# Kernel optimization log

Hardware: AMD Instinct MI355X
Metric: run time of the kernel (lower is better)

The kernel has to match this reference:

```python
import jax, jax.numpy as jnp
import numpy as np

N_CH, LONG, LAT = 8, 64, 64
N = N_CH * LONG * LAT          # 32768 flattened node count
OUT = 16 * 16                  # output_size ** 2
BATCH = 512


def _build_adjacency(n, long_, lat):
    # Faithful reconstruction of the (intended) COO pattern in GNNLayer.__init__.
    rows, cols, vals = [], [], []
    for k in range(n):
        for j in range(0, long_ * lat, 3):
            rows += [k + j, k + j, j]
            cols += [k + j, j, k + j]
            vals += [1.0, 1.0, 1.0]
        for i in range(lat + 1, (long_ - 1) * lat - 1, 3):
            offs = [i - 1, i + 1, i + lat, i - lat,
                    i + lat - 1, i + lat + 1, i - lat - 1, i - lat + 1]
            for o in offs:
                rows.append(i); cols.append(k + o); vals.append(1.0)
            for o in offs:
                rows.append(k + o); cols.append(i); vals.append(1.0)
    return (np.asarray(rows, np.int32), np.asarray(cols, np.int32),
            np.asarray(vals, np.float32))


def setup_inputs() -> dict:
    key = jax.random.key(0)
    k1, k2, k3 = jax.random.split(key, 3)
    rows, cols, vals = _build_adjacency(N_CH, LONG, LAT)
    x = jax.random.normal(k1, (BATCH, N_CH, LONG, LAT), jnp.float32)
    W = jax.random.normal(k2, (OUT, N), jnp.float32) / np.sqrt(N)  # lin1.weight
    b = jax.random.normal(k3, (OUT,), jnp.float32) * 0.01          # lin1.bias
    return {"x": x, "W": W, "b": b,
            "vals": jnp.asarray(vals),
            "rows": jnp.asarray(rows), "cols": jnp.asarray(cols)}


def reference(x, W, b, vals, rows, cols):
    B = x.shape[0]
    xf = x.reshape(B, -1)                    # [B, N]
    # SpMM with duplicate-index accumulation (matches torch COO coalescing):
    gathered = xf[:, cols] * vals            # [B, nnz]
    h1 = jax.ops.segment_sum(gathered.T, rows, num_segments=N).T  # [B, N]
    return h1 @ W.T + b                      # [B, 256]
```

## Files before the change

### kernel.cpp

```cpp
#include <hip/hip_runtime.h>
#include <hip/hip_bf16.h>

#define N_NODES 32768
#define OUT_F   256
#define BATCH   512
#define ROWS_CAP 4352
#define KS       17
#define KSLICE   256
#define NSTEP    (KSLICE / 32)
#define GBM 64
#define GBN 64
#define FOLD_BLOCKS (KS * OUT_F)
#define OUT_BLOCKS  ((BATCH * OUT_F) / 256)
#define HALO 72
#define WIN  400


typedef __attribute__((ext_vector_type(8))) short short8;
typedef __attribute__((ext_vector_type(4))) float f32x4;

__device__ __forceinline__ float bf2f(ushort u) {
    return __uint_as_float(((unsigned)u) << 16);
}
__device__ __forceinline__ ushort f2bf(float f) {
    unsigned u = __float_as_uint(f);
    return (ushort)((u + 0x7fffu + ((u >> 16) & 1u)) >> 16);
}
__device__ __forceinline__ bool inJ(int x) { return x >= 0 && x <= 4095 && x % 3 == 0; }
__device__ __forceinline__ bool inI(int x) { return x >= 65 && x <= 4028 && x % 3 == 2; }

__global__ __launch_bounds__(256) void k_fused(const float* __restrict__ W,
                                               const float* __restrict__ bias,
                                               ushort* __restrict__ wbf2,
                                               float* __restrict__ out) {
    __shared__ float lw[WIN];
    int bid = blockIdx.x, t = threadIdx.x;
    if (bid < FOLD_BLOCKS) {
        int chunk = bid >> 8;
        int o     = bid & 255;
        int c0    = chunk * 256;
        int rbase = c0 - HALO;
        const float* wrow = W + (long)o * N_NODES;
        if (t < WIN / 4) {
            int r = rbase + t * 4;
            float4 v = (r >= 0) ? *(const float4*)(wrow + r)
                                : make_float4(0.f, 0.f, 0.f, 0.f);
            *(float4*)(lw + t * 4) = v;
        }
        __syncthreads();
        const int soff[30] = {-65,-64,-63,-62,-61,-60,-59,-58,-57,-56,
                               -1,  0,  1,  2,  3,  4,  5,  6,  7,  8,
                               63, 64, 65, 66, 67, 68, 69, 70, 71, 72};
        const float smul[30] = {1,2,3,3,3,3,3,3,2,1,
                                1,1,2,2,2,2,2,2,1,1,
                                1,2,3,3,3,3,3,3,2,1};
        int c = c0 + t;
        int ci = t + HALO;
        float accJ = 0.f, accI = 0.f;
        int m1 = 0;
        #pragma unroll
        for (int k = 0; k < 8; ++k) {
            int j = c - k;
            if (inJ(j)) { ++m1; accJ += lw[ci - k]; }
        }
        if (m1) accJ += (float)m1 * lw[ci];
        if (inJ(c)) {
            #pragma unroll
            for (int k = 0; k < 8; ++k) accJ += lw[ci + k];
        }
        #pragma unroll
        for (int q = 0; q < 30; ++q) {
            if (inI(c - soff[q])) accI += smul[q] * lw[ci - soff[q]];
        }
        if (inI(c)) {
            #pragma unroll
            for (int q = 0; q < 30; ++q) accI += smul[q] * lw[ci + soff[q]];
        }
        wbf2[(long)o * ROWS_CAP + c] = f2bf(accJ + accI);
        return;
    }
    int idx = (bid - FOLD_BLOCKS) * 256 + t;
    out[idx] = bias[idx & (OUT_F - 1)];
}

__global__ __launch_bounds__(256) void k_gemm(const float* __restrict__ xf,
                                              const ushort* __restrict__ wbf2,
                                              float* __restrict__ out) {
    __shared__ ushort Ash[2][GBM * 40];
    __shared__ ushort Bsh[2][GBN * 40];
    int t = threadIdx.x;
    int w = t >> 6, lane = t & 63;
    int lrow = lane & 15, lseg = lane >> 4;
    int gm0 = blockIdx.x * GBM, gn0 = blockIdx.y * GBN, k0 = blockIdx.z * KSLICE;
    int row = t >> 2, kc = (t & 3) * 8;
    const float*  pa = xf   + (long)(gm0 + row) * N_NODES  + k0 + kc;
    const ushort* pb = wbf2 + (long)(gn0 + row) * ROWS_CAP + k0 + kc;

    {
        float4 x0 = *(const float4*)(pa);
        float4 x1 = *(const float4*)(pa + 4);
        short8 va;
        va[0] = (short)f2bf(x0.x); va[1] = (short)f2bf(x0.y);
        va[2] = (short)f2bf(x0.z); va[3] = (short)f2bf(x0.w);
        va[4] = (short)f2bf(x1.x); va[5] = (short)f2bf(x1.y);
        va[6] = (short)f2bf(x1.z); va[7] = (short)f2bf(x1.w);
        *(short8*)(Ash[0] + row * 40 + kc) = va;
        *(short8*)(Bsh[0] + row * 40 + kc) = *(const short8*)(pb);
    }
    __syncthreads();

    f32x4 acc[4] = {};
    for (int ks = 0; ks < NSTEP; ++ks) {
        int cur = ks & 1;
        bool more = (ks + 1) < NSTEP;
        float4 x0, x1; short8 vb;
        if (more) {
            x0 = *(const float4*)(pa + (ks + 1) * 32);
            x1 = *(const float4*)(pa + (ks + 1) * 32 + 4);
            vb = *(const short8*)(pb + (ks + 1) * 32);
        }
        short8 af = *(const short8*)(Ash[cur] + (w * 16 + lrow) * 40 + lseg * 8);
        #pragma unroll
        for (int f = 0; f < 4; ++f) {
            short8 bf = *(const short8*)(Bsh[cur] + (f * 16 + lrow) * 40 + lseg * 8);
            acc[f] = __builtin_amdgcn_mfma_f32_16x16x32_bf16(af, bf, acc[f], 0, 0, 0);
        }
        if (more) {
            short8 va;
            va[0] = (short)f2bf(x0.x); va[1] = (short)f2bf(x0.y);
            va[2] = (short)f2bf(x0.z); va[3] = (short)f2bf(x0.w);
            va[4] = (short)f2bf(x1.x); va[5] = (short)f2bf(x1.y);
            va[6] = (short)f2bf(x1.z); va[7] = (short)f2bf(x1.w);
            *(short8*)(Ash[cur ^ 1] + row * 40 + kc) = va;
            *(short8*)(Bsh[cur ^ 1] + row * 40 + kc) = vb;
        }
        __syncthreads();
    }
    #pragma unroll
    for (int f = 0; f < 4; ++f)
        #pragma unroll
        for (int i = 0; i < 4; ++i) {
            int rowg = gm0 + w * 16 + lseg * 4 + i;
            int colg = gn0 + f * 16 + lrow;
            atomicAdd(&out[(long)rowg * OUT_F + colg], acc[f][i]);
        }
}

extern "C" void kernel_launch(void* const* d_in, const int* in_sizes, int n_in,
                              void* d_out, int out_size, void* d_ws, size_t ws_size,
                              hipStream_t stream) {
    const float* xf   = (const float*)d_in[0];
    const float* W    = (const float*)d_in[1];
    const float* bias = (const float*)d_in[2];

    ushort* wbf2 = (ushort*)d_ws;

    k_fused<<<FOLD_BLOCKS + OUT_BLOCKS, 256, 0, stream>>>(W, bias, wbf2, (float*)d_out);

    k_gemm<<<dim3(BATCH / GBM, OUT_F / GBN, KS), 256, 0, stream>>>(xf, wbf2, (float*)d_out);
}
```

Measured before the change: 30.71 us.

## Replace split-K atomic accumulation with partial buffers and a separate reduce kernel

The GEMM no longer atomically adds each split-K slice into the output. Each slice now writes its partial tile to a workspace buffer, and a new reduce kernel sums the 17 partials and adds the bias. Bias initialisation moves out of the fold kernel. This removes atomic contention, at the cost of an extra kernel launch and about 9 MB of partial-buffer writes and reads.

```diff
diff --git a/kernel.cpp b/kernel.cpp
--- a/kernel.cpp
+++ b/kernel.cpp
@@ -11,7 +11,7 @@
 #define GBM 64
 #define GBN 64
 #define FOLD_BLOCKS (KS * OUT_F)
-#define OUT_BLOCKS  ((BATCH * OUT_F) / 256)
+#define RED_BLOCKS  ((BATCH * OUT_F) / 256)
 #define HALO 72
 #define WIN  400
 
@@ -29,63 +29,56 @@
 __device__ __forceinline__ bool inJ(int x) { return x >= 0 && x <= 4095 && x % 3 == 0; }
 __device__ __forceinline__ bool inI(int x) { return x >= 65 && x <= 4028 && x % 3 == 2; }
 
-__global__ __launch_bounds__(256) void k_fused(const float* __restrict__ W,
-                                               const float* __restrict__ bias,
-                                               ushort* __restrict__ wbf2,
-                                               float* __restrict__ out) {
+__global__ __launch_bounds__(256) void k_fold(const float* __restrict__ W,
+                                              ushort* __restrict__ wbf2) {
     __shared__ float lw[WIN];
     int bid = blockIdx.x, t = threadIdx.x;
-    if (bid < FOLD_BLOCKS) {
-        int chunk = bid >> 8;
-        int o     = bid & 255;
-        int c0    = chunk * 256;
-        int rbase = c0 - HALO;
-        const float* wrow = W + (long)o * N_NODES;
-        if (t < WIN / 4) {
-            int r = rbase + t * 4;
-            float4 v = (r >= 0) ? *(const float4*)(wrow + r)
-                                : make_float4(0.f, 0.f, 0.f, 0.f);
-            *(float4*)(lw + t * 4) = v;
-        }
-        __syncthreads();
-        const int soff[30] = {-65,-64,-63,-62,-61,-60,-59,-58,-57,-56,
-                               -1,  0,  1,  2,  3,  4,  5,  6,  7,  8,
-                               63, 64, 65, 66, 67, 68, 69, 70, 71, 72};
-        const float smul[30] = {1,2,3,3,3,3,3,3,2,1,
-                                1,1,2,2,2,2,2,2,1,1,
-                                1,2,3,3,3,3,3,3,2,1};
-        int c = c0 + t;
-        int ci = t + HALO;
-        float accJ = 0.f, accI = 0.f;
-        int m1 = 0;
+    int chunk = bid >> 8;
+    int o     = bid & 255;
+    int c0    = chunk * 256;
+    int rbase = c0 - HALO;
+    const float* wrow = W + (long)o * N_NODES;
+    if (t < WIN / 4) {
+        int r = rbase + t * 4;
+        float4 v = (r >= 0) ? *(const float4*)(wrow + r)
+                            : make_float4(0.f, 0.f, 0.f, 0.f);
+        *(float4*)(lw + t * 4) = v;
+    }
+    __syncthreads();
+    const int soff[30] = {-65,-64,-63,-62,-61,-60,-59,-58,-57,-56,
+                           -1,  0,  1,  2,  3,  4,  5,  6,  7,  8,
+                           63, 64, 65, 66, 67, 68, 69, 70, 71, 72};
+    const float smul[30] = {1,2,3,3,3,3,3,3,2,1,
+                            1,1,2,2,2,2,2,2,1,1,
+                            1,2,3,3,3,3,3,3,2,1};
+    int c = c0 + t;
+    int ci = t + HALO;
+    float accJ = 0.f, accI = 0.f;
+    int m1 = 0;
+    #pragma unroll
+    for (int k = 0; k < 8; ++k) {
+        int j = c - k;
+        if (inJ(j)) { ++m1; accJ += lw[ci - k]; }
+    }
+    if (m1) accJ += (float)m1 * lw[ci];
+    if (inJ(c)) {
         #pragma unroll
-        for (int k = 0; k < 8; ++k) {
-            int j = c - k;
-            if (inJ(j)) { ++m1; accJ += lw[ci - k]; }
-        }
-        if (m1) accJ += (float)m1 * lw[ci];
-        if (inJ(c)) {
-            #pragma unroll
-            for (int k = 0; k < 8; ++k) accJ += lw[ci + k];
-        }
+        for (int k = 0; k < 8; ++k) accJ += lw[ci + k];
+    }
+    #pragma unroll
+    for (int q = 0; q < 30; ++q) {
+        if (inI(c - soff[q])) accI += smul[q] * lw[ci - soff[q]];
+    }
+    if (inI(c)) {
         #pragma unroll
-        for (int q = 0; q < 30; ++q) {
-            if (inI(c - soff[q])) accI += smul[q] * lw[ci - soff[q]];
-        }
-        if (inI(c)) {
-            #pragma unroll
-            for (int q = 0; q < 30; ++q) accI += smul[q] * lw[ci + soff[q]];
-        }
-        wbf2[(long)o * ROWS_CAP + c] = f2bf(accJ + accI);
-        return;
+        for (int q = 0; q < 30; ++q) accI += smul[q] * lw[ci + soff[q]];
     }
-    int idx = (bid - FOLD_BLOCKS) * 256 + t;
-    out[idx] = bias[idx & (OUT_F - 1)];
+    wbf2[(long)o * ROWS_CAP + c] = f2bf(accJ + accI);
 }
 
 __global__ __launch_bounds__(256) void k_gemm(const float* __restrict__ xf,
                                               const ushort* __restrict__ wbf2,
-                                              float* __restrict__ out) {
+                                              float* __restrict__ partial) {
     __shared__ ushort Ash[2][GBM * 40];
     __shared__ ushort Bsh[2][GBN * 40];
     int t = threadIdx.x;
@@ -136,14 +129,26 @@
         }
         __syncthreads();
     }
+    float* dst = partial + (long)blockIdx.z * BATCH * OUT_F;
     #pragma unroll
     for (int f = 0; f < 4; ++f)
         #pragma unroll
         for (int i = 0; i < 4; ++i) {
             int rowg = gm0 + w * 16 + lseg * 4 + i;
             int colg = gn0 + f * 16 + lrow;
-            atomicAdd(&out[(long)rowg * OUT_F + colg], acc[f][i]);
+            dst[(long)rowg * OUT_F + colg] = acc[f][i];
         }
+}
+
+__global__ __launch_bounds__(256) void k_reduce(const float* __restrict__ partial,
+                                                const float* __restrict__ bias,
+                                                float* __restrict__ out) {
+    int idx = blockIdx.x * 256 + threadIdx.x;
+    float s = bias[idx & (OUT_F - 1)];
+    #pragma unroll
+    for (int z = 0; z < KS; ++z)
+        s += partial[(long)z * BATCH * OUT_F + idx];
+    out[idx] = s;
 }
 
 extern "C" void kernel_launch(void* const* d_in, const int* in_sizes, int n_in,
@@ -153,9 +158,13 @@
     const float* W    = (const float*)d_in[1];
     const float* bias = (const float*)d_in[2];
 
-    ushort* wbf2 = (ushort*)d_ws;
+    char* base = (char*)d_ws;
+    ushort* wbf2 = (ushort*)base;
+    float* partial = (float*)(base + (size_t)OUT_F * ROWS_CAP * sizeof(ushort));
 
-    k_fused<<<FOLD_BLOCKS + OUT_BLOCKS, 256, 0, stream>>>(W, bias, wbf2, (float*)d_out);
+    k_fold<<<FOLD_BLOCKS, 256, 0, stream>>>(W, wbf2);
 
-    k_gemm<<<dim3(BATCH / GBM, OUT_F / GBN, KS), 256, 0, stream>>>(xf, wbf2, (float*)d_out);
+    k_gemm<<<dim3(BATCH / GBM, OUT_F / GBN, KS), 256, 0, stream>>>(xf, wbf2, partial);
+
+    k_reduce<<<RED_BLOCKS, 256, 0, stream>>>(partial, bias, (float*)d_out);
 }
```

Result: faster. 29.22 us (-4.8%).
